# Performance work log

Hardware: AMD Instinct MI355X
Metric: run time of the kernel (lower is better)

The kernel has to match this reference:

```python
import jax, jax.numpy as jnp
import numpy as np

WINDOW = 5
D_CONV = 4
HEADDIM = 64
NGROUPS = 1
EPS = 1e-5


def _silu(x):
    return x * jax.nn.sigmoid(x)


def _causal_dwconv(x, w, b):
    # x: (B, L, C), w: (C, K), b: (C,) -- depthwise causal conv along L
    K = w.shape[1]
    L = x.shape[1]
    xp = jnp.pad(x, ((0, 0), (K - 1, 0), (0, 0)))
    y = b
    for k in range(K):
        y = y + xp[:, k:k + L, :] * w[:, k]
    return y


def _mamba2_layer(x, in_w, cw, cb, dtb, A_log, Dh, nw, ow):
    # x: (B, L, dim). Mamba2 mixer (mamba_ssm defaults: ngroups=1, rmsnorm gated, no proj bias)
    B, L, _ = x.shape
    d_inner = nw.shape[0]
    nheads = dtb.shape[0]
    p = d_inner // nheads
    conv_dim = cw.shape[0]
    n = (conv_dim - d_inner) // 2  # d_state
    zxbcdt = x @ in_w.T  # (B, L, 2*d_inner + 2*n + nheads)
    z, xBC, dt = jnp.split(zxbcdt, [d_inner, d_inner + conv_dim], axis=-1)
    dt = jax.nn.softplus(dt + dtb)  # (B, L, h)
    xBC = _silu(_causal_dwconv(xBC, cw, cb))
    xh, Bm, Cm = jnp.split(xBC, [d_inner, d_inner + n], axis=-1)
    xh = xh.reshape(B, L, nheads, p)
    A = -jnp.exp(A_log)  # (h,)

    def step(h, inp):
        dt_t, x_t, B_t, C_t = inp  # (B,h), (B,h,p), (B,n), (B,n)
        decay = jnp.exp(dt_t * A)  # (B,h)
        h = h * decay[..., None, None] + (dt_t[..., None] * x_t)[..., None] * B_t[:, None, None, :]
        y = jnp.einsum('bhpn,bn->bhp', h, C_t)
        return h, y

    h0 = jnp.zeros((B, nheads, p, n), x.dtype)
    _, ys = jax.lax.scan(step, h0, (dt.transpose(1, 0, 2), xh.transpose(1, 0, 2, 3),
                                    Bm.transpose(1, 0, 2), Cm.transpose(1, 0, 2)))
    y = ys.transpose(1, 0, 2, 3) + Dh[None, None, :, None] * xh  # (B, L, h, p)
    y = y.reshape(B, L, d_inner)
    # gated RMSNorm (norm_before_gate=False): gate then normalize
    y = y * _silu(z)
    y = y * jax.lax.rsqrt(jnp.mean(y * y, axis=-1, keepdims=True) + EPS) * nw
    return y @ ow.T


def setup_inputs() -> dict:
    key = jax.random.key(0)
    ks = iter(jax.random.split(key, 24))
    B, T, C = 8, 2048, 3
    dim, depth, d_state, expand = 128, 4, 64, 2
    d_inner = expand * dim
    nheads = d_inner // HEADDIM
    conv_dim = d_inner + 2 * NGROUPS * d_state
    d_in_proj = 2 * d_inner + 2 * NGROUPS * d_state + nheads
    nrm = lambda shp, s=1.0: jax.random.normal(next(ks), shp, jnp.float32) * s
    return {
        'x': nrm((B, T, C)),
        'mlp_w1': nrm((128, C * WINDOW), 0.2), 'mlp_b1': jnp.zeros((128,), jnp.float32),
        'mlp_w2': nrm((dim, 128), 0.1), 'mlp_b2': jnp.zeros((dim,), jnp.float32),
        'cls_token': nrm((1, 1, dim)),
        'in_proj_w': nrm((depth, d_in_proj, dim), 0.05),
        'conv_w': nrm((depth, conv_dim, D_CONV), 0.3),
        'conv_b': jnp.zeros((depth, conv_dim), jnp.float32),
        'dt_bias': nrm((depth, nheads), 0.5),
        'A_log': jnp.log(jax.random.uniform(next(ks), (depth, nheads), jnp.float32, 1.0, 16.0)),
        'Dh': jnp.ones((depth, nheads), jnp.float32),
        'norm_w': jnp.ones((depth, d_inner), jnp.float32),
        'out_proj_w': nrm((depth, dim, d_inner), 0.05),
        'ln_w': jnp.ones((dim,), jnp.float32), 'ln_b': jnp.zeros((dim,), jnp.float32),
        'head_w': nrm((1, dim), 0.1), 'head_b': jnp.zeros((1,), jnp.float32),
    }


def reference(x, mlp_w1, mlp_b1, mlp_w2, mlp_b2, cls_token, in_proj_w, conv_w, conv_b,
              dt_bias, A_log, Dh, norm_w, out_proj_w, ln_w, ln_b, head_w, head_b):
    B, T, C = x.shape
    L = T - WINDOW + 1
    # Unfold + rearrange 'b (c w) l -> b l (w c)' == sliding windows flattened (window outer, channel inner)
    tok = jnp.stack([x[:, k:k + L, :] for k in range(WINDOW)], axis=2).reshape(B, L, WINDOW * C)
    h = jax.nn.gelu(tok @ mlp_w1.T + mlp_b1, approximate=False) @ mlp_w2.T + mlp_b2
    dim = h.shape[-1]
    h = jnp.concatenate([h, jnp.broadcast_to(cls_token, (B, 1, dim))], axis=1)
    for i in range(in_proj_w.shape[0]):
        h = _mamba2_layer(h, in_proj_w[i], conv_w[i], conv_b[i], dt_bias[i],
                          A_log[i], Dh[i], norm_w[i], out_proj_w[i])
    cls = h[:, -1]
    mu = jnp.mean(cls, axis=-1, keepdims=True)
    var = jnp.mean((cls - mu) ** 2, axis=-1, keepdims=True)
    cls_n = (cls - mu) * jax.lax.rsqrt(var + 1e-5) * ln_w + ln_b
    out = (cls_n @ head_w.T + head_b)[:, 0]
    return out, h
```

## Files before the change

### kernel.cpp

```cpp
#include <hip/hip_runtime.h>
#include <math.h>

#define BATCH 8
#define TSEQ 2048
#define CIN 3
#define WIN 5
#define LSEQ 2044
#define LH 2045
#define DIM 128
#define DEPTH 4
#define DIN 256
#define NH 4
#define PDIM 64
#define NSTATE 64
#define CONVD 384
#define DPROJ 644
#define NJT 41
#define QC 64
#define NCH 32
#define LDS2 68
#define LDSY 268
#define LDSH 140
#define FTR 32
#define OTOK 32

typedef __attribute__((ext_vector_type(8))) short bf16x8;
typedef __attribute__((ext_vector_type(4))) float f32x4;
union Frag8 { bf16x8 v; uint2 u[2]; };

__device__ __forceinline__ float sigmoidf_(float x){ return 1.f/(1.f+__expf(-x)); }
__device__ __forceinline__ float siluf_(float x){ return x*sigmoidf_(x); }
__device__ __forceinline__ unsigned short f2bf(float f){
  unsigned int u = __float_as_uint(f);
  return (unsigned short)((u + 0x7FFFu + ((u >> 16) & 1u)) >> 16);
}
__device__ __forceinline__ float bf2f(unsigned short u){
  return __uint_as_float(((unsigned int)u) << 16);
}
__device__ __forceinline__ unsigned int pack2(float a, float b){
  return (unsigned int)f2bf(a) | ((unsigned int)f2bf(b) << 16);
}
__device__ __forceinline__ unsigned int pack2lo(float a, float b){
  float ra = a - bf2f(f2bf(a)), rb = b - bf2f(f2bf(b));
  return (unsigned int)f2bf(ra) | ((unsigned int)f2bf(rb) << 16);
}
__device__ __forceinline__ bf16x8 ldfrag(const unsigned short* base, int off){
  Frag8 f;
  f.u[0] = *(const uint2*)(base + off);
  f.u[1] = *(const uint2*)(base + off + 4);
  return f.v;
}

__global__ void __launch_bounds__(256) k_cast_all(
    const float* __restrict__ w, const float* __restrict__ ow,
    unsigned short* __restrict__ wH, unsigned short* __restrict__ wL,
    unsigned short* __restrict__ oH, unsigned short* __restrict__ oL) {
  int blk = blockIdx.x;
  if (blk < 164) {
    int gid = blk*256 + threadIdx.x;
    int lane = gid & 63;
    int kb = (gid >> 6) & 3;
    int jt = (gid >> 8) % NJT;
    int ly = gid / (NJT*4*64);
    int m = lane & 15, q = lane >> 4;
    int j = jt*16 + m;
    int k = kb*32 + q*8;
    unsigned short hi[8], lo[8];
    if (j < DPROJ) {
      const float* src = w + ((size_t)ly*DPROJ + j)*DIM + k;
#pragma unroll
      for (int i = 0; i < 8; ++i) {
        float v = src[i];
        hi[i] = f2bf(v);
        lo[i] = f2bf(v - bf2f(hi[i]));
      }
    } else {
#pragma unroll
      for (int i = 0; i < 8; ++i) { hi[i] = 0; lo[i] = 0; }
    }
    size_t dst = (size_t)gid*8;
    *(uint4*)(wH + dst) = *(const uint4*)hi;
    *(uint4*)(wL + dst) = *(const uint4*)lo;
  } else {
    int gid = (blk - 164)*256 + threadIdx.x;
    int lane = gid & 63;
    int kb = (gid >> 6) & 7;
    int jt = (gid >> 9) & 7;
    int ly = gid >> 12;
    int m = lane & 15, q = lane >> 4;
    int j = jt*16 + m;
    int k = kb*32 + q*8;
    const float* src = ow + ((size_t)ly*DIM + j)*DIN + k;
    unsigned short hi[8], lo[8];
#pragma unroll
    for (int i = 0; i < 8; ++i) {
      float v = src[i];
      hi[i] = f2bf(v);
      lo[i] = f2bf(v - bf2f(hi[i]));
    }
    size_t dst = (size_t)gid*8;
    *(uint4*)(oH + dst) = *(const uint4*)hi;
    *(uint4*)(oL + dst) = *(const uint4*)lo;
  }
}

__global__ void __launch_bounds__(512) k_front_proj(
    const float* __restrict__ x, const float* __restrict__ w1,
    const float* __restrict__ b1, const float* __restrict__ w2,
    const float* __restrict__ b2, const float* __restrict__ cls,
    const unsigned short* __restrict__ wH, const unsigned short* __restrict__ wL,
    const float* __restrict__ dtb, float* __restrict__ zx) {
  int t = threadIdx.x;
  int b = blockIdx.x >> 6;
  int c0 = (blockIdx.x & 63) * FTR;
  __shared__ __align__(16) float pool[108 + 2176 + 4096 + 8192];
  float* xs   = pool;
  float* w1s  = pool + 108;
  float* h1s  = pool + 108 + 2176;
  float* part = pool + 108 + 2176 + 4096;
  unsigned short* hsH = (unsigned short*)pool;
  unsigned short* hsL = hsH + 32*LDSH;
  for (int i = t; i < (FTR+4)*CIN; i += 512) {
    int row = c0 + i/3, ch = i - (i/3)*3;
    xs[i] = (row < TSEQ) ? x[(size_t)b*TSEQ*CIN + (size_t)row*CIN + ch] : 0.f;
  }
  for (int i = t; i < DIM*15; i += 512) {
    int j = i/15, k = i - j*15;
    w1s[j*17+k] = w1[i];
  }
  __syncthreads();
  {
    int j = t & 127, rh = t >> 7;
    float bias = b1[j];
    const float* wr = &w1s[j*17];
    for (int r = rh*8; r < rh*8+8; ++r) {
      float a = bias;
#pragma unroll
      for (int k = 0; k < 15; ++k) a += xs[r*3+k]*wr[k];
      h1s[r*128 + j] = 0.5f*a*(1.f + erff(a*0.70710678118654752f));
    }
  }
  __syncthreads();
  {
    int j = t & 127, z = t >> 7;
    int hf = z & 1, rh2 = z >> 1;
    float4 wv[16];
    const float4* w2r = (const float4*)(w2 + (size_t)j*DIM + hf*64);
#pragma unroll
    for (int k4 = 0; k4 < 16; ++k4) wv[k4] = w2r[k4];
#pragma unroll 2
    for (int r = rh2*16; r < rh2*16+16; ++r) {
      const float4* hr = (const float4*)&h1s[r*128 + hf*64];
      float acc = 0.f;
#pragma unroll
      for (int k4 = 0; k4 < 16; ++k4) {
        float4 hv = hr[k4];
        acc += wv[k4].x*hv.x + wv[k4].y*hv.y + wv[k4].z*hv.z + wv[k4].w*hv.w;
      }
      part[(r*128 + j)*2 + hf] = acc;
    }
  }
  __syncthreads();
  {
    int c = t & 127, rh = t >> 7;
    float bias = b2[c];
    for (int r = rh*8; r < rh*8+8; ++r) {
      int l = c0 + r;
      float val;
      if (l < LSEQ)       val = part[(r*128 + c)*2] + part[(r*128 + c)*2 + 1] + bias;
      else if (l == LSEQ) val = cls[c];
      else                val = 0.f;
      unsigned short hi = f2bf(val);
      hsH[r*LDSH + c] = hi;
      hsL[r*LDSH + c] = f2bf(val - bf2f(hi));
    }
  }
  __syncthreads();
  int wave = t >> 6, lane = t & 63;
  int m = lane & 15, q = lane >> 4;
#pragma unroll 2
  for (int jt = wave; jt < NJT; jt += 8) {
    size_t woff = (((size_t)jt*4)*64 + lane)*8;
    bf16x8 bh[4], bl[4];
#pragma unroll
    for (int kb = 0; kb < 4; ++kb) {
      bh[kb] = *(const bf16x8*)(wH + woff + (size_t)kb*64*8);
      bl[kb] = *(const bf16x8*)(wL + woff + (size_t)kb*64*8);
    }
    f32x4 acc0 = {0.f, 0.f, 0.f, 0.f}, acc1 = {0.f, 0.f, 0.f, 0.f};
#pragma unroll
    for (int kb = 0; kb < 4; ++kb) {
      int o0 = m*LDSH + kb*32 + q*8;
      int o1 = (16 + m)*LDSH + kb*32 + q*8;
      bf16x8 a0h = ldfrag(hsH, o0), a0l = ldfrag(hsL, o0);
      bf16x8 a1h = ldfrag(hsH, o1), a1l = ldfrag(hsL, o1);
      acc0 = __builtin_amdgcn_mfma_f32_16x16x32_bf16(a0l, bh[kb], acc0, 0, 0, 0);
      acc0 = __builtin_amdgcn_mfma_f32_16x16x32_bf16(a0h, bl[kb], acc0, 0, 0, 0);
      acc0 = __builtin_amdgcn_mfma_f32_16x16x32_bf16(a0h, bh[kb], acc0, 0, 0, 0);
      acc1 = __builtin_amdgcn_mfma_f32_16x16x32_bf16(a1l, bh[kb], acc1, 0, 0, 0);
      acc1 = __builtin_amdgcn_mfma_f32_16x16x32_bf16(a1h, bl[kb], acc1, 0, 0, 0);
      acc1 = __builtin_amdgcn_mfma_f32_16x16x32_bf16(a1h, bh[kb], acc1, 0, 0, 0);
    }
    int jj = jt*16 + m;
    if (jj < DPROJ) {
      bool isdt = (jj >= 640);
      float bias = isdt ? dtb[jj - 640] : 0.f;
#pragma unroll
      for (int r = 0; r < 4; ++r) {
        int tok = c0 + q*4 + r;
        if (tok < LH) {
          float vv = acc0[r];
          if (isdt) { vv += bias; vv = (vv > 20.f) ? vv : log1pf(__expf(vv)); }
          zx[((size_t)b*LH + tok)*DPROJ + jj] = vv;
        }
        int tok1 = c0 + 16 + q*4 + r;
        if (tok1 < LH) {
          float vv = acc1[r];
          if (isdt) { vv += bias; vv = (vv > 20.f) ? vv : log1pf(__expf(vv)); }
          zx[((size_t)b*LH + tok1)*DPROJ + jj] = vv;
        }
      }
    }
  }
}

__global__ void k_conv(const float* __restrict__ zx, const float* __restrict__ cw,
                       const float* __restrict__ cb, float* __restrict__ xbc) {
  size_t idx = (size_t)blockIdx.x*blockDim.x + threadIdx.x;
  const size_t total = (size_t)BATCH*LH*(CONVD/4);
  if (idx >= total) return;
  int c4 = (int)(idx % (CONVD/4)) * 4;
  size_t bl = idx / (CONVD/4);
  int l = (int)(bl % LH); int b = (int)(bl / LH);
  float4 w0 = *(const float4*)(cw + (c4+0)*4);
  float4 w1 = *(const float4*)(cw + (c4+1)*4);
  float4 w2 = *(const float4*)(cw + (c4+2)*4);
  float4 w3 = *(const float4*)(cw + (c4+3)*4);
  float4 a = *(const float4*)(cb + c4);
#pragma unroll
  for (int k = 0; k < 4; ++k) {
    int tin = l - 3 + k;
    if (tin >= 0) {
      float4 v = *(const float4*)(zx + ((size_t)b*LH + tin)*DPROJ + DIN + c4);
      a.x += v.x * ((const float*)&w0)[k];
      a.y += v.y * ((const float*)&w1)[k];
      a.z += v.z * ((const float*)&w2)[k];
      a.w += v.w * ((const float*)&w3)[k];
    }
  }
  float4 o;
  o.x = siluf_(a.x); o.y = siluf_(a.y); o.z = siluf_(a.z); o.w = siluf_(a.w);
  *(float4*)(xbc + ((size_t)b*LH + l)*CONVD + c4) = o;
}

__global__ void __launch_bounds__(512, 8) k_chunk_state(
    const float* __restrict__ zx, const float* __restrict__ xbc,
    const float* __restrict__ A_log, float* __restrict__ G, float* __restrict__ dec) {
  int blk = blockIdx.x;
  int c = blk & (NCH-1), hd = (blk >> 5) & 3, b = blk >> 7;
  int t0 = c*QC;
  int tid = threadIdx.x;
  int wave = tid >> 6, lane = tid & 63;
  int wr = wave & 3, wh = wave >> 2;
  int m = lane & 15, q = lane >> 4;
  float A = -__expf(A_log[hd]);
  __shared__ __align__(16) unsigned short BcH[QC*LDS2], BcL[QC*LDS2];
  __shared__ __align__(16) unsigned short XtH[QC*LDS2], XtL[QC*LDS2];
  __shared__ float coef[QC];
  float dtv = 0.f;
  if (tid < 64) {
    int tg = t0 + tid;
    dtv = (tg < LH) ? zx[((size_t)b*LH + tg)*DPROJ + 640 + hd] : 0.f;
  }
  float pb[8], px[8];
#pragma unroll
  for (int it = 0; it < 4; ++it) {
    int i = tid + it*512;
    int n = i & 63, s2 = (i >> 6)*2;
    int tg0 = t0 + s2, tg1 = tg0 + 1;
    float b0 = 0.f, b1 = 0.f, x0 = 0.f, x1 = 0.f;
    if (tg0 < LH) {
      size_t row = ((size_t)b*LH + tg0)*CONVD;
      b0 = xbc[row + DIN + n];
      x0 = xbc[row + hd*PDIM + n];
    }
    if (tg1 < LH) {
      size_t row = ((size_t)b*LH + tg1)*CONVD;
      b1 = xbc[row + DIN + n];
      x1 = xbc[row + hd*PDIM + n];
    }
    pb[it*2] = b0; pb[it*2+1] = b1; px[it*2] = x0; px[it*2+1] = x1;
  }
  if (tid < 64) {
    float s = dtv;
#pragma unroll
    for (int off = 1; off < 64; off <<= 1) {
      float u = __shfl_up(s, off);
      if (tid >= off) s += u;
    }
    float cq = __shfl(s, 63);
    coef[tid] = __expf(A*(cq - s)) * dtv;
    if (tid == 63) dec[blk] = __expf(A * s);
  }
  __syncthreads();
#pragma unroll
  for (int it = 0; it < 4; ++it) {
    int i = tid + it*512;
    int n = i & 63, s2 = (i >> 6)*2;
    float c0_ = coef[s2], c1_ = coef[s2+1];
    float b0 = pb[it*2]*c0_, b1 = pb[it*2+1]*c1_;
    float x0 = px[it*2],     x1 = px[it*2+1];
    int o = n*LDS2 + s2;
    *(unsigned int*)(BcH + o) = pack2(b0, b1);
    *(unsigned int*)(BcL + o) = pack2lo(b0, b1);
    *(unsigned int*)(XtH + o) = pack2(x0, x1);
    *(unsigned int*)(XtL + o) = pack2lo(x0, x1);
  }
  __syncthreads();
  bf16x8 ah[2], al[2];
#pragma unroll
  for (int kc = 0; kc < 2; ++kc) {
    int off = (wr*16 + m)*LDS2 + kc*32 + q*8;
    ah[kc] = ldfrag(BcH, off);
    al[kc] = ldfrag(BcL, off);
  }
#pragma unroll
  for (int nth = 0; nth < 2; ++nth) {
    int nt = wh*2 + nth;
    f32x4 acc = {0.f,0.f,0.f,0.f};
#pragma unroll
    for (int kc = 0; kc < 2; ++kc) {
      int off = (nt*16 + m)*LDS2 + kc*32 + q*8;
      bf16x8 xh = ldfrag(XtH, off), xl = ldfrag(XtL, off);
      acc = __builtin_amdgcn_mfma_f32_16x16x32_bf16(al[kc], xh, acc, 0, 0, 0);
      acc = __builtin_amdgcn_mfma_f32_16x16x32_bf16(ah[kc], xl, acc, 0, 0, 0);
      acc = __builtin_amdgcn_mfma_f32_16x16x32_bf16(ah[kc], xh, acc, 0, 0, 0);
    }
    int p = nt*16 + m;
#pragma unroll
    for (int r = 0; r < 4; ++r) {
      int n = wr*16 + q*4 + r;
      G[(size_t)blk*4096 + n*64 + p] = acc[r];
    }
  }
}

__global__ void __launch_bounds__(256) k_combine(
    const float* __restrict__ G, const float* __restrict__ dec, float* __restrict__ Hin) {
  int bh = blockIdx.x >> 2, esp = blockIdx.x & 3;
  int e = esp*1024 + threadIdx.x*4;
  size_t base0 = (size_t)bh*NCH*4096 + e;
  float4 gq[4]; float dq[4];
#pragma unroll
  for (int k = 0; k < 4; ++k) {
    gq[k] = *(const float4*)(G + base0 + (size_t)k*4096);
    dq[k] = dec[bh*NCH + k];
  }
  float4 H = make_float4(0.f,0.f,0.f,0.f);
#pragma unroll 4
  for (int c = 0; c < NCH; ++c) {
    int slot = c & 3;
    float4 g = gq[slot]; float d = dq[slot];
    if (c + 4 < NCH) {
      gq[slot] = *(const float4*)(G + base0 + (size_t)(c+4)*4096);
      dq[slot] = dec[bh*NCH + c + 4];
    }
    *(float4*)(Hin + base0 + (size_t)c*4096) = H;
    H.x = H.x*d + g.x; H.y = H.y*d + g.y; H.z = H.z*d + g.z; H.w = H.w*d + g.w;
  }
}

__global__ void __launch_bounds__(512, 8) k_chunk_out(
    const float* __restrict__ zx, const float* __restrict__ xbc,
    const float* __restrict__ A_log, const float* __restrict__ Hin,
    float* __restrict__ y) {
  int blk = blockIdx.x;
  int c = blk & (NCH-1), hd = (blk >> 5) & 3, b = blk >> 7;
  int t0 = c*QC;
  int tid = threadIdx.x;
  int wave = tid >> 6, lane = tid & 63;
  int wr = wave & 3, wh = wave >> 2;
  int m = lane & 15, q = lane >> 4;
  float A = -__expf(A_log[hd]);
  __shared__ __align__(16) unsigned short P0H[QC*LDS2], P0L[QC*LDS2];
  __shared__ __align__(16) unsigned short P1H[QC*LDS2], P1L[QC*LDS2];
  __shared__ float cum[QC], dts[QC], pref[QC];
  float dtv = 0.f;
  if (tid < 64) {
    int tg = t0 + tid;
    dtv = (tg < LH) ? zx[((size_t)b*LH + tg)*DPROJ + 640 + hd] : 0.f;
  }
  float pbv[8], pcv[8];
#pragma unroll
  for (int it = 0; it < 4; ++it) {
    int i = tid + it*512;
    int s = i >> 5, j2 = (i & 31)*2;
    int tg = t0 + s;
    float b0 = 0.f, b1 = 0.f, c0_ = 0.f, c1_ = 0.f;
    if (tg < LH) {
      size_t row = ((size_t)b*LH + tg)*CONVD;
      float2 bv = *(const float2*)(xbc + row + DIN + j2);
      float2 cv = *(const float2*)(xbc + row + DIN + NSTATE + j2);
      b0 = bv.x; b1 = bv.y; c0_ = cv.x; c1_ = cv.y;
    }
    pbv[it*2] = b0; pbv[it*2+1] = b1; pcv[it*2] = c0_; pcv[it*2+1] = c1_;
  }
  size_t hbase = (size_t)blk*4096;
  float hv[8];
#pragma unroll
  for (int it = 0; it < 4; ++it) {
    int i = tid + it*512;
    int p = i & 63, n2 = (i >> 6)*2;
    hv[it*2]   = Hin[hbase + (size_t)n2*64 + p];
    hv[it*2+1] = Hin[hbase + (size_t)(n2+1)*64 + p];
  }
  if (tid < 64) {
    float s = dtv;
#pragma unroll
    for (int off = 1; off < 64; off <<= 1) {
      float u = __shfl_up(s, off);
      if (tid >= off) s += u;
    }
    dts[tid] = dtv; cum[tid] = s; pref[tid] = __expf(A*s);
  }
#pragma unroll
  for (int it = 0; it < 4; ++it) {
    int i = tid + it*512;
    int s = i >> 5, j2 = (i & 31)*2;
    int o = s*LDS2 + j2;
    *(unsigned int*)(P1H + o) = pack2(pbv[it*2], pbv[it*2+1]);
    *(unsigned int*)(P1L + o) = pack2lo(pbv[it*2], pbv[it*2+1]);
    *(unsigned int*)(P0H + o) = pack2(pcv[it*2], pcv[it*2+1]);
    *(unsigned int*)(P0L + o) = pack2lo(pcv[it*2], pcv[it*2+1]);
  }
  __syncthreads();
  bf16x8 ch[2], cl[2];
#pragma unroll
  for (int kc = 0; kc < 2; ++kc) {
    int off = (wr*16 + m)*LDS2 + kc*32 + q*8;
    ch[kc] = ldfrag(P0H, off);
    cl[kc] = ldfrag(P0L, off);
  }
  f32x4 sacc[2];
#pragma unroll
  for (int nth = 0; nth < 2; ++nth) {
    int nt = wh*2 + nth;
    f32x4 a1 = {0.f,0.f,0.f,0.f};
#pragma unroll
    for (int kc = 0; kc < 2; ++kc) {
      int off = (nt*16 + m)*LDS2 + kc*32 + q*8;
      bf16x8 bh = ldfrag(P1H, off), bl = ldfrag(P1L, off);
      a1 = __builtin_amdgcn_mfma_f32_16x16x32_bf16(cl[kc], bh, a1, 0, 0, 0);
      a1 = __builtin_amdgcn_mfma_f32_16x16x32_bf16(ch[kc], bl, a1, 0, 0, 0);
      a1 = __builtin_amdgcn_mfma_f32_16x16x32_bf16(ch[kc], bh, a1, 0, 0, 0);
    }
    sacc[nth] = a1;
  }
  __syncthreads();
  float xv[8];
#pragma unroll
  for (int it = 0; it < 4; ++it) {
    int i = tid + it*512;
    int p = i & 63, s2 = (i >> 6)*2;
    int tg = t0 + s2;
    xv[it*2]   = (tg < LH)   ? xbc[((size_t)b*LH + tg)*CONVD + hd*PDIM + p]   : 0.f;
    xv[it*2+1] = (tg+1 < LH) ? xbc[((size_t)b*LH + tg+1)*CONVD + hd*PDIM + p] : 0.f;
  }
#pragma unroll
  for (int nth = 0; nth < 2; ++nth) {
    int nt = wh*2 + nth;
    int s = nt*16 + m;
#pragma unroll
    for (int r = 0; r < 4; ++r) {
      int t = wr*16 + q*4 + r;
      float mv = 0.f;
      if (s <= t) mv = sacc[nth][r] * __expf(A*(cum[t] - cum[s])) * dts[s];
      unsigned short hi = f2bf(mv);
      P0H[t*LDS2 + s] = hi;
      P0L[t*LDS2 + s] = f2bf(mv - bf2f(hi));
    }
  }
#pragma unroll
  for (int it = 0; it < 4; ++it) {
    int i = tid + it*512;
    int p = i & 63, n2 = (i >> 6)*2;
    int o = p*LDS2 + n2;
    *(unsigned int*)(P1H + o) = pack2(hv[it*2], hv[it*2+1]);
    *(unsigned int*)(P1L + o) = pack2lo(hv[it*2], hv[it*2+1]);
  }
  __syncthreads();
  f32x4 y2a[2];
#pragma unroll
  for (int nth = 0; nth < 2; ++nth) {
    int nt = wh*2 + nth;
    f32x4 a2 = {0.f,0.f,0.f,0.f};
#pragma unroll
    for (int kc = 0; kc < 2; ++kc) {
      int off = (nt*16 + m)*LDS2 + kc*32 + q*8;
      bf16x8 th = ldfrag(P1H, off), tl = ldfrag(P1L, off);
      a2 = __builtin_amdgcn_mfma_f32_16x16x32_bf16(cl[kc], th, a2, 0, 0, 0);
      a2 = __builtin_amdgcn_mfma_f32_16x16x32_bf16(ch[kc], tl, a2, 0, 0, 0);
      a2 = __builtin_amdgcn_mfma_f32_16x16x32_bf16(ch[kc], th, a2, 0, 0, 0);
    }
    y2a[nth] = a2;
  }
  bf16x8 mh[2], ml[2];
#pragma unroll
  for (int kc = 0; kc < 2; ++kc) {
    int off = (wr*16 + m)*LDS2 + kc*32 + q*8;
    mh[kc] = ldfrag(P0H, off);
    ml[kc] = ldfrag(P0L, off);
  }
  __syncthreads();
#pragma unroll
  for (int it = 0; it < 4; ++it) {
    int i = tid + it*512;
    int p = i & 63, s2 = (i >> 6)*2;
    int o = p*LDS2 + s2;
    *(unsigned int*)(P1H + o) = pack2(xv[it*2], xv[it*2+1]);
    *(unsigned int*)(P1L + o) = pack2lo(xv[it*2], xv[it*2+1]);
  }
  __syncthreads();
#pragma unroll
  for (int nth = 0; nth < 2; ++nth) {
    int nt = wh*2 + nth;
    f32x4 a1 = {0.f,0.f,0.f,0.f};
#pragma unroll
    for (int kc = 0; kc < 2; ++kc) {
      int off = (nt*16 + m)*LDS2 + kc*32 + q*8;
      bf16x8 th = ldfrag(P1H, off), tl = ldfrag(P1L, off);
      a1 = __builtin_amdgcn_mfma_f32_16x16x32_bf16(ml[kc], th, a1, 0, 0, 0);
      a1 = __builtin_amdgcn_mfma_f32_16x16x32_bf16(mh[kc], tl, a1, 0, 0, 0);
      a1 = __builtin_amdgcn_mfma_f32_16x16x32_bf16(mh[kc], th, a1, 0, 0, 0);
    }
    int p = nt*16 + m;
#pragma unroll
    for (int r = 0; r < 4; ++r) {
      int t = wr*16 + q*4 + r, tg = t0 + t;
      if (tg < LH)
        y[((size_t)b*LH + tg)*DIN + hd*PDIM + p] = a1[r] + pref[t]*y2a[nth][r];
    }
  }
}

__global__ void __launch_bounds__(512, 4) k_out_fused(
    const float* __restrict__ y, const float* __restrict__ xbc,
    float* __restrict__ zx, const float* __restrict__ Dh,
    const float* __restrict__ nw, const unsigned short* __restrict__ oH,
    const unsigned short* __restrict__ oL,
    const unsigned short* __restrict__ wH, const unsigned short* __restrict__ wL,
    const float* __restrict__ dtb, float* __restrict__ hout, int doProj) {
  int b = blockIdx.x >> 6;
  int l0 = (blockIdx.x & 63) * OTOK;
  int t = threadIdx.x;
  __shared__ __align__(16) unsigned short yH[OTOK*LDSY], yL[OTOK*LDSY];
  __shared__ __align__(16) unsigned short hsH[OTOK*LDSH], hsL[OTOK*LDSH];
  __shared__ float red[OTOK][4];
  __shared__ float rs[OTOK];
  int wave = t >> 6, lane = t & 63;
  bf16x8 pwh[4], pwl[4];
#pragma unroll
  for (int kb = 0; kb < 4; ++kb) {
    size_t woff = (((size_t)wave*8 + kb)*64 + lane)*8;
    pwh[kb] = *(const bf16x8*)(oH + woff);
    pwl[kb] = *(const bf16x8*)(oL + woff);
  }
  int c = t & 255;
  int rh = t >> 8;
  int r0 = rh*16;
  int hd = c >> 6;
  float dcoef = Dh[hd];
  float nwc = nw[c];
  float v[16];
#pragma unroll
  for (int r = 0; r < 16; ++r) {
    int l = l0 + r0 + r;
    float val = 0.f;
    if (l < LH) {
      size_t row = (size_t)b*LH + l;
      float ys = y[row*DIN + c];
      float xh = xbc[row*CONVD + c];
      float z  = zx[row*DPROJ + c];
      val = (ys + dcoef*xh) * siluf_(z);
    }
    v[r] = val;
  }
  int qw = wave & 3;
#pragma unroll
  for (int r = 0; r < 16; ++r) {
    float sq = v[r]*v[r];
    for (int off = 32; off > 0; off >>= 1) sq += __shfl_down(sq, off);
    if (lane == 0) red[r0 + r][qw] = sq;
  }
  __syncthreads();
  if (t < OTOK) {
    float sm = red[t][0]+red[t][1]+red[t][2]+red[t][3];
    rs[t] = rsqrtf(sm/(float)DIN + 1e-5f);
  }
  __syncthreads();
#pragma unroll
  for (int r = 0; r < 16; ++r) {
    float val = v[r] * rs[r0 + r] * nwc;
    unsigned short hi = f2bf(val);
    yH[(r0 + r)*LDSY + c] = hi;
    yL[(r0 + r)*LDSY + c] = f2bf(val - bf2f(hi));
  }
  __syncthreads();
  int m = lane & 15, q = lane >> 4;
  {
    int jt = wave;
    f32x4 acc0 = {0.f,0.f,0.f,0.f}, acc1 = {0.f,0.f,0.f,0.f};
#pragma unroll
    for (int kb = 0; kb < 8; ++kb) {
      bf16x8 bh, bl;
      if (kb < 4) { bh = pwh[kb]; bl = pwl[kb]; }
      else {
        size_t woff = (((size_t)jt*8 + kb)*64 + lane)*8;
        bh = *(const bf16x8*)(oH + woff);
        bl = *(const bf16x8*)(oL + woff);
      }
      int o0 = m*LDSY + kb*32 + q*8;
      int o1 = (16 + m)*LDSY + kb*32 + q*8;
      bf16x8 a0h = ldfrag(yH, o0), a0l = ldfrag(yL, o0);
      bf16x8 a1h = ldfrag(yH, o1), a1l = ldfrag(yL, o1);
      acc0 = __builtin_amdgcn_mfma_f32_16x16x32_bf16(a0l, bh, acc0, 0, 0, 0);
      acc0 = __builtin_amdgcn_mfma_f32_16x16x32_bf16(a0h, bl, acc0, 0, 0, 0);
      acc0 = __builtin_amdgcn_mfma_f32_16x16x32_bf16(a0h, bh, acc0, 0, 0, 0);
      acc1 = __builtin_amdgcn_mfma_f32_16x16x32_bf16(a1l, bh, acc1, 0, 0, 0);
      acc1 = __builtin_amdgcn_mfma_f32_16x16x32_bf16(a1h, bl, acc1, 0, 0, 0);
      acc1 = __builtin_amdgcn_mfma_f32_16x16x32_bf16(a1h, bh, acc1, 0, 0, 0);
    }
    int j = jt*16 + m;
#pragma unroll
    for (int r = 0; r < 4; ++r) {
      int rr = q*4 + r;
      float val = acc0[r];
      unsigned short hi = f2bf(val);
      hsH[rr*LDSH + j] = hi;
      hsL[rr*LDSH + j] = f2bf(val - bf2f(hi));
      int l = l0 + rr;
      if (!doProj && l < LH) hout[((size_t)b*LH + l)*DIM + j] = val;
      int rr1 = 16 + q*4 + r;
      float val1 = acc1[r];
      unsigned short hi1 = f2bf(val1);
      hsH[rr1*LDSH + j] = hi1;
      hsL[rr1*LDSH + j] = f2bf(val1 - bf2f(hi1));
      int l1 = l0 + rr1;
      if (!doProj && l1 < LH) hout[((size_t)b*LH + l1)*DIM + j] = val1;
    }
  }
  if (!doProj) return;
  __syncthreads();
#pragma unroll 2
  for (int jt = wave; jt < NJT; jt += 8) {
    size_t woff = (((size_t)jt*4)*64 + lane)*8;
    bf16x8 bh[4], bl[4];
#pragma unroll
    for (int kb = 0; kb < 4; ++kb) {
      bh[kb] = *(const bf16x8*)(wH + woff + (size_t)kb*64*8);
      bl[kb] = *(const bf16x8*)(wL + woff + (size_t)kb*64*8);
    }
    f32x4 acc0 = {0.f, 0.f, 0.f, 0.f}, acc1 = {0.f, 0.f, 0.f, 0.f};
#pragma unroll
    for (int kb = 0; kb < 4; ++kb) {
      int o0 = m*LDSH + kb*32 + q*8;
      int o1 = (16 + m)*LDSH + kb*32 + q*8;
      bf16x8 a0h = ldfrag(hsH, o0), a0l = ldfrag(hsL, o0);
      bf16x8 a1h = ldfrag(hsH, o1), a1l = ldfrag(hsL, o1);
      acc0 = __builtin_amdgcn_mfma_f32_16x16x32_bf16(a0l, bh[kb], acc0, 0, 0, 0);
      acc0 = __builtin_amdgcn_mfma_f32_16x16x32_bf16(a0h, bl[kb], acc0, 0, 0, 0);
      acc0 = __builtin_amdgcn_mfma_f32_16x16x32_bf16(a0h, bh[kb], acc0, 0, 0, 0);
      acc1 = __builtin_amdgcn_mfma_f32_16x16x32_bf16(a1l, bh[kb], acc1, 0, 0, 0);
      acc1 = __builtin_amdgcn_mfma_f32_16x16x32_bf16(a1h, bl[kb], acc1, 0, 0, 0);
      acc1 = __builtin_amdgcn_mfma_f32_16x16x32_bf16(a1h, bh[kb], acc1, 0, 0, 0);
    }
    int jj = jt*16 + m;
    if (jj < DPROJ) {
      bool isdt = (jj >= 640);
      float bias = isdt ? dtb[jj - 640] : 0.f;
#pragma unroll
      for (int r = 0; r < 4; ++r) {
        int tok = l0 + q*4 + r;
        if (tok < LH) {
          float vv = acc0[r];
          if (isdt) { vv += bias; vv = (vv > 20.f) ? vv : log1pf(__expf(vv)); }
          zx[((size_t)b*LH + tok)*DPROJ + jj] = vv;
        }
        int tok1 = l0 + 16 + q*4 + r;
        if (tok1 < LH) {
          float vv = acc1[r];
          if (isdt) { vv += bias; vv = (vv > 20.f) ? vv : log1pf(__expf(vv)); }
          zx[((size_t)b*LH + tok1)*DPROJ + jj] = vv;
        }
      }
    }
  }
}

__global__ void k_head(const float* __restrict__ h, const float* __restrict__ lnw,
                       const float* __restrict__ lnb, const float* __restrict__ hw,
                       const float* __restrict__ hb, float* __restrict__ out) {
  int b = blockIdx.x; int t = threadIdx.x;
  __shared__ float red[2];
  int wave = t >> 6, lane = t & 63;
  float v = h[((size_t)b*LH + LSEQ)*DIM + t];
  float s = v;
  for (int off = 32; off > 0; off >>= 1) s += __shfl_down(s, off);
  if (lane == 0) red[wave] = s;
  __syncthreads();
  float mean = (red[0]+red[1]) / (float)DIM;
  __syncthreads();
  float d = v - mean; float sq = d*d;
  for (int off = 32; off > 0; off >>= 1) sq += __shfl_down(sq, off);
  if (lane == 0) red[wave] = sq;
  __syncthreads();
  float var = (red[0]+red[1]) / (float)DIM;
  float cn = d*rsqrtf(var + 1e-5f)*lnw[t] + lnb[t];
  float dot = cn*hw[t];
  __syncthreads();
  for (int off = 32; off > 0; off >>= 1) dot += __shfl_down(dot, off);
  if (lane == 0) red[wave] = dot;
  __syncthreads();
  if (t == 0) out[b] = red[0]+red[1] + hb[0];
}

extern "C" void kernel_launch(void* const* d_in, const int* in_sizes, int n_in,
                              void* d_out, int out_size, void* d_ws, size_t ws_size,
                              hipStream_t stream) {
  const float* x     = (const float*)d_in[0];
  const float* w1    = (const float*)d_in[1];
  const float* b1    = (const float*)d_in[2];
  const float* w2    = (const float*)d_in[3];
  const float* b2    = (const float*)d_in[4];
  const float* cls   = (const float*)d_in[5];
  const float* inw   = (const float*)d_in[6];
  const float* cw    = (const float*)d_in[7];
  const float* cb    = (const float*)d_in[8];
  const float* dtb   = (const float*)d_in[9];
  const float* Alog  = (const float*)d_in[10];
  const float* Dh    = (const float*)d_in[11];
  const float* nw    = (const float*)d_in[12];
  const float* ow    = (const float*)d_in[13];
  const float* lnw   = (const float*)d_in[14];
  const float* lnb   = (const float*)d_in[15];
  const float* hw    = (const float*)d_in[16];
  const float* hb    = (const float*)d_in[17];

  float* ws   = (float*)d_ws;
  float* zx   = ws;
  float* xbc  = zx + (size_t)BATCH*LH*DPROJ;
  float* ybuf = xbc + (size_t)BATCH*LH*CONVD;
  float* G    = ybuf;
  float* Hin  = ybuf + 4194304;
  float* dec  = Hin  + 4194304;
  unsigned short* wH = (unsigned short*)(dec + 1024);
  unsigned short* wL = wH + (size_t)DEPTH*NJT*4*64*8;
  unsigned short* oH = wL + (size_t)DEPTH*NJT*4*64*8;
  unsigned short* oL = oH + (size_t)DEPTH*8*8*64*8;

  float* hout = (float*)d_out + 8;

  k_cast_all<<<228, 256, 0, stream>>>(inw, ow, wH, wL, oH, oL);

  k_front_proj<<<BATCH*64, 512, 0, stream>>>(x, w1, b1, w2, b2, cls,
                                             wH, wL, dtb, zx);

  for (int i = 0; i < DEPTH; ++i) {
    int doProj = (i < DEPTH-1) ? 1 : 0;
    int nxt = doProj ? (i+1) : 0;
    k_conv<<<(int)(((long)BATCH*LH*(CONVD/4) + 255)/256), 256, 0, stream>>>(
        zx, cw + (size_t)i*CONVD*4, cb + (size_t)i*CONVD, xbc);
    k_chunk_state<<<BATCH*NH*NCH, 512, 0, stream>>>(zx, xbc, Alog + i*NH, G, dec);
    k_combine<<<BATCH*NH*4, 256, 0, stream>>>(G, dec, Hin);
    k_chunk_out<<<BATCH*NH*NCH, 512, 0, stream>>>(zx, xbc, Alog + i*NH, Hin, ybuf);
    k_out_fused<<<BATCH*64, 512, 0, stream>>>(
        ybuf, xbc, zx, Dh + i*NH, nw + (size_t)i*DIN,
        oH + (size_t)i*8*8*64*8, oL + (size_t)i*8*8*64*8,
        wH + (size_t)nxt*NJT*4*64*8, wL + (size_t)nxt*NJT*4*64*8,
        dtb + nxt*NH, hout, doProj);
  }

  k_head<<<BATCH, 128, 0, stream>>>(hout, lnw, lnb, hw, hb, (float*)d_out);
}
```

Baseline: 469.9 us.

## Fuse causal depthwise conv into chunk-state kernel and drop separate conv launch

The separate causal conv + SiLU kernel is removed. Each chunk-state block now computes the conv for its own head's x channels and the B channels directly from zx, writing the bf16 split fragments to LDS and also storing xbc for later kernels. The hd==1 blocks additionally compute and store the C channels. This saves one launch per layer and a full read of xbc in chunk_state. In exchange it adds redundant B conv work across heads, serial per-thread conv loops with strided global loads, and a lower occupancy bound.

Result: faster. 429.4 us (-8.6%).

```diff
diff --git a/kernel.cpp b/kernel.cpp
--- a/kernel.cpp
+++ b/kernel.cpp
@@ -224,38 +224,10 @@
   }
 }
 
-__global__ void k_conv(const float* __restrict__ zx, const float* __restrict__ cw,
-                       const float* __restrict__ cb, float* __restrict__ xbc) {
-  size_t idx = (size_t)blockIdx.x*blockDim.x + threadIdx.x;
-  const size_t total = (size_t)BATCH*LH*(CONVD/4);
-  if (idx >= total) return;
-  int c4 = (int)(idx % (CONVD/4)) * 4;
-  size_t bl = idx / (CONVD/4);
-  int l = (int)(bl % LH); int b = (int)(bl / LH);
-  float4 w0 = *(const float4*)(cw + (c4+0)*4);
-  float4 w1 = *(const float4*)(cw + (c4+1)*4);
-  float4 w2 = *(const float4*)(cw + (c4+2)*4);
-  float4 w3 = *(const float4*)(cw + (c4+3)*4);
-  float4 a = *(const float4*)(cb + c4);
-#pragma unroll
-  for (int k = 0; k < 4; ++k) {
-    int tin = l - 3 + k;
-    if (tin >= 0) {
-      float4 v = *(const float4*)(zx + ((size_t)b*LH + tin)*DPROJ + DIN + c4);
-      a.x += v.x * ((const float*)&w0)[k];
-      a.y += v.y * ((const float*)&w1)[k];
-      a.z += v.z * ((const float*)&w2)[k];
-      a.w += v.w * ((const float*)&w3)[k];
-    }
-  }
-  float4 o;
-  o.x = siluf_(a.x); o.y = siluf_(a.y); o.z = siluf_(a.z); o.w = siluf_(a.w);
-  *(float4*)(xbc + ((size_t)b*LH + l)*CONVD + c4) = o;
-}
-
-__global__ void __launch_bounds__(512, 8) k_chunk_state(
-    const float* __restrict__ zx, const float* __restrict__ xbc,
-    const float* __restrict__ A_log, float* __restrict__ G, float* __restrict__ dec) {
+__global__ void __launch_bounds__(512, 4) k_chunk_state(
+    const float* __restrict__ zx, const float* __restrict__ cw,
+    const float* __restrict__ cb, const float* __restrict__ A_log,
+    float* __restrict__ G, float* __restrict__ dec, float* __restrict__ xbc) {
   int blk = blockIdx.x;
   int c = blk & (NCH-1), hd = (blk >> 5) & 3, b = blk >> 7;
   int t0 = c*QC;
@@ -272,24 +244,65 @@
     int tg = t0 + tid;
     dtv = (tg < LH) ? zx[((size_t)b*LH + tg)*DPROJ + 640 + hd] : 0.f;
   }
-  float pb[8], px[8];
-#pragma unroll
-  for (int it = 0; it < 4; ++it) {
-    int i = tid + it*512;
-    int n = i & 63, s2 = (i >> 6)*2;
-    int tg0 = t0 + s2, tg1 = tg0 + 1;
-    float b0 = 0.f, b1 = 0.f, x0 = 0.f, x1 = 0.f;
-    if (tg0 < LH) {
-      size_t row = ((size_t)b*LH + tg0)*CONVD;
-      b0 = xbc[row + DIN + n];
-      x0 = xbc[row + hd*PDIM + n];
-    }
-    if (tg1 < LH) {
-      size_t row = ((size_t)b*LH + tg1)*CONVD;
-      b1 = xbc[row + DIN + n];
-      x1 = xbc[row + hd*PDIM + n];
-    }
-    pb[it*2] = b0; pb[it*2+1] = b1; px[it*2] = x0; px[it*2+1] = x1;
+  int chIdx = tid & 127, half = tid >> 7;
+  bool isB = (chIdx >= 64);
+  int n = chIdx & 63;
+  int xch = isB ? (DIN + n) : (hd*PDIM + n);
+  int col = 256 + xch;
+  const float4 wv4 = *(const float4*)(cw + xch*4);
+  float bias = cb[xch];
+  int s0 = half*16;
+  float bb[16];
+  {
+    float x3, x2, x1;
+    int t3 = t0 + s0 - 3, t2_ = t0 + s0 - 2, t1_ = t0 + s0 - 1;
+    x3 = (t3 >= 0 && t3 < LH) ? zx[((size_t)b*LH + t3)*DPROJ + col] : 0.f;
+    x2 = (t2_ >= 0 && t2_ < LH) ? zx[((size_t)b*LH + t2_)*DPROJ + col] : 0.f;
+    x1 = (t1_ >= 0 && t1_ < LH) ? zx[((size_t)b*LH + t1_)*DPROJ + col] : 0.f;
+    float prev = 0.f;
+#pragma unroll
+    for (int i = 0; i < 16; ++i) {
+      int s = s0 + i;
+      int tg = t0 + s;
+      float x0 = (tg < LH) ? zx[((size_t)b*LH + tg)*DPROJ + col] : 0.f;
+      float a = bias;
+      a += x3*wv4.x; a += x2*wv4.y; a += x1*wv4.z; a += x0*wv4.w;
+      float out = (tg < LH) ? siluf_(a) : 0.f;
+      if (tg < LH && (!isB || hd == 0))
+        xbc[((size_t)b*LH + tg)*CONVD + xch] = out;
+      if (isB) {
+        bb[i] = out;
+      } else {
+        if (i & 1) {
+          int o = n*LDS2 + (s - 1);
+          *(unsigned int*)(XtH + o) = pack2(prev, out);
+          *(unsigned int*)(XtL + o) = pack2lo(prev, out);
+        } else prev = out;
+      }
+      x3 = x2; x2 = x1; x1 = x0;
+    }
+  }
+  if (hd == 1) {
+    int cc = tid & 63, oct = tid >> 6;
+    int xch2 = DIN + NSTATE + cc;
+    int col2 = 256 + xch2;
+    const float4 w2v = *(const float4*)(cw + xch2*4);
+    float bias2 = cb[xch2];
+    int s0c = oct*8;
+    float x3, x2, x1;
+    int t3 = t0 + s0c - 3, t2_ = t0 + s0c - 2, t1_ = t0 + s0c - 1;
+    x3 = (t3 >= 0 && t3 < LH) ? zx[((size_t)b*LH + t3)*DPROJ + col2] : 0.f;
+    x2 = (t2_ >= 0 && t2_ < LH) ? zx[((size_t)b*LH + t2_)*DPROJ + col2] : 0.f;
+    x1 = (t1_ >= 0 && t1_ < LH) ? zx[((size_t)b*LH + t1_)*DPROJ + col2] : 0.f;
+#pragma unroll
+    for (int i = 0; i < 8; ++i) {
+      int tg = t0 + s0c + i;
+      float x0 = (tg < LH) ? zx[((size_t)b*LH + tg)*DPROJ + col2] : 0.f;
+      float a = bias2;
+      a += x3*w2v.x; a += x2*w2v.y; a += x1*w2v.z; a += x0*w2v.w;
+      if (tg < LH) xbc[((size_t)b*LH + tg)*CONVD + xch2] = siluf_(a);
+      x3 = x2; x2 = x1; x1 = x0;
+    }
   }
   if (tid < 64) {
     float s = dtv;
@@ -303,18 +316,16 @@
     if (tid == 63) dec[blk] = __expf(A * s);
   }
   __syncthreads();
-#pragma unroll
-  for (int it = 0; it < 4; ++it) {
-    int i = tid + it*512;
-    int n = i & 63, s2 = (i >> 6)*2;
-    float c0_ = coef[s2], c1_ = coef[s2+1];
-    float b0 = pb[it*2]*c0_, b1 = pb[it*2+1]*c1_;
-    float x0 = px[it*2],     x1 = px[it*2+1];
-    int o = n*LDS2 + s2;
-    *(unsigned int*)(BcH + o) = pack2(b0, b1);
-    *(unsigned int*)(BcL + o) = pack2lo(b0, b1);
-    *(unsigned int*)(XtH + o) = pack2(x0, x1);
-    *(unsigned int*)(XtL + o) = pack2lo(x0, x1);
+  if (isB) {
+#pragma unroll
+    for (int j = 0; j < 8; ++j) {
+      int s = s0 + 2*j;
+      float b0 = bb[2*j]   * coef[s];
+      float b1 = bb[2*j+1] * coef[s+1];
+      int o = n*LDS2 + s;
+      *(unsigned int*)(BcH + o) = pack2(b0, b1);
+      *(unsigned int*)(BcL + o) = pack2lo(b0, b1);
+    }
   }
   __syncthreads();
   bf16x8 ah[2], al[2];
@@ -339,8 +350,8 @@
     int p = nt*16 + m;
 #pragma unroll
     for (int r = 0; r < 4; ++r) {
-      int n = wr*16 + q*4 + r;
-      G[(size_t)blk*4096 + n*64 + p] = acc[r];
+      int n2 = wr*16 + q*4 + r;
+      G[(size_t)blk*4096 + n2*64 + p] = acc[r];
     }
   }
 }
@@ -768,9 +779,8 @@
   for (int i = 0; i < DEPTH; ++i) {
     int doProj = (i < DEPTH-1) ? 1 : 0;
     int nxt = doProj ? (i+1) : 0;
-    k_conv<<<(int)(((long)BATCH*LH*(CONVD/4) + 255)/256), 256, 0, stream>>>(
-        zx, cw + (size_t)i*CONVD*4, cb + (size_t)i*CONVD, xbc);
-    k_chunk_state<<<BATCH*NH*NCH, 512, 0, stream>>>(zx, xbc, Alog + i*NH, G, dec);
+    k_chunk_state<<<BATCH*NH*NCH, 512, 0, stream>>>(
+        zx, cw + (size_t)i*CONVD*4, cb + (size_t)i*CONVD, Alog + i*NH, G, dec, xbc);
     k_combine<<<BATCH*NH*4, 256, 0, stream>>>(G, dec, Hin);
     k_chunk_out<<<BATCH*NH*NCH, 512, 0, stream>>>(zx, xbc, Alog + i*NH, Hin, ybuf);
     k_out_fused<<<BATCH*64, 512, 0, stream>>>(
```
